# Optimization experiments

Measured on AMD Instinct MI355X. Metric: run time of the kernel, lower is better.

The kernel has to match this reference:

```python
import jax, jax.numpy as jnp
import numpy as np

B, L, K = 4, 2048, 30
HID, EDGE, NL, NH = 128, 16, 3, 4
HD = HID // NH
SCALE = HD ** -0.5
LN_EPS = 1e-5


def setup_inputs() -> dict:
    key = jax.random.key(0)
    ks = jax.random.split(key, 16)
    s = 0.05
    d = {
        "h_nodes": jax.random.normal(ks[0], (B, L, HID), jnp.float32),
        "h_edges": jax.random.normal(ks[1], (B, L, K, EDGE), jnp.float32),
        "mask": jnp.ones((B, L), jnp.float32),
        "Wq": jax.random.normal(ks[2], (NL, HID, HID), jnp.float32) * s,
        "bq": jax.random.normal(ks[3], (NL, HID), jnp.float32) * s,
        "Wk": jax.random.normal(ks[4], (NL, HID, HID), jnp.float32) * s,
        "bk": jax.random.normal(ks[5], (NL, HID), jnp.float32) * s,
        "Wv": jax.random.normal(ks[6], (NL, HID, HID), jnp.float32) * s,
        "bv": jax.random.normal(ks[7], (NL, HID), jnp.float32) * s,
        "We": jax.random.normal(ks[8], (NL, EDGE, NH), jnp.float32) * s,
        "be": jax.random.normal(ks[9], (NL, NH), jnp.float32) * s,
        "Wo": jax.random.normal(ks[10], (NL, HID, HID), jnp.float32) * s,
        "bo": jax.random.normal(ks[11], (NL, HID), jnp.float32) * s,
        "ln_g": jnp.ones((NL, HID), jnp.float32),
        "ln_b": jnp.zeros((NL, HID), jnp.float32),
        "edge_idxs": jax.random.randint(ks[12], (B, L, K), 0, L, jnp.int32),
    }
    return d


def _layer_norm(x, g, b):
    mu = jnp.mean(x, axis=-1, keepdims=True)
    var = jnp.mean((x - mu) ** 2, axis=-1, keepdims=True)
    return (x - mu) * jax.lax.rsqrt(var + LN_EPS) * g + b


# per-batch gather of rows: a [L, ...], idx [L, K] -> [L, K, ...]
_gather = jax.vmap(lambda a, i: a[i])


def _forward(h_nodes, h_edges, mask, Wq, bq, Wk, bk, Wv, bv, We, be, Wo, bo, ln_g, ln_b, edge_idxs):
    neigh_mask = _gather(mask, edge_idxs)                     # [B,L,K]
    attn_mask = mask[:, None, :, None] * neigh_mask[:, None]  # [B,1,L,K]
    h = h_nodes
    for i in range(NL):
        hn = _gather(h, edge_idxs)                            # [B,L,K,HID]
        q = (h @ Wq[i] + bq[i]).reshape(B, L, NH, HD)
        k = (hn @ Wk[i] + bk[i]).reshape(B, L, K, NH, HD)
        v = (hn @ Wv[i] + bv[i]).reshape(B, L, K, NH, HD)
        scores = jnp.einsum('blhd,blkhd->bhlk', q, k) * SCALE
        scores = scores + jnp.transpose(h_edges @ We[i] + be[i], (0, 3, 1, 2))  # edge bias [B,NH,L,K]
        scores = jnp.where(attn_mask == 0, -1e9, scores)
        w = jax.nn.softmax(scores, axis=-1)                   # [B,NH,L,K]
        o = jnp.einsum('bhlk,blkhd->blhd', w, v).reshape(B, L, HID)
        o = o @ Wo[i] + bo[i]
        h = _layer_norm(h + o, ln_g[i], ln_b[i]) * mask[..., None]
    return h


def reference(h_nodes, h_edges, edge_idxs, mask, Wq, bq, Wk, bk, Wv, bv, We, be, Wo, bo, ln_g, ln_b):
    return _forward(h_nodes, h_edges, mask, Wq, bq, Wk, bk, Wv, bv, We, be, Wo, bo, ln_g, ln_b, edge_idxs)
```

## Files before the change

### kernel.cpp

```cpp
#include <hip/hip_runtime.h>
#include <math.h>

#define BB 4
#define LL 2048
#define KK 30
#define HIDD 128
#define EDGEE 16
#define NLL 3
#define NHH 4
#define SCALE_ 0.17677669529663687f
#define NROW 8192
#define NEDG 245760

typedef __attribute__((ext_vector_type(8))) short bf16x8;
typedef __attribute__((ext_vector_type(4))) float f32x4;

__device__ __forceinline__ ushort f2b(float f) {
    union { float f; uint u; } x; x.f = f;
    uint r = x.u + 0x7fff + ((x.u >> 16) & 1);
    return (ushort)(r >> 16);
}

__global__ __launch_bounds__(256) void prep_kernel(
    const float* __restrict__ Wq, const float* __restrict__ Wk,
    const float* __restrict__ Wv, const float* __restrict__ Wo,
    const float* __restrict__ h_edges, const float* __restrict__ We,
    const float* __restrict__ be, const float* __restrict__ h_nodes,
    ushort* __restrict__ WbT, float* __restrict__ eb, ushort* __restrict__ hb)
{
    const int id = blockIdx.x * 256 + threadIdx.x;
    if (blockIdx.y == 0) {
        if (id < 12 * 128 * 128) {
            int m = id >> 14;
            int rem = id & 16383;
            int k = rem >> 7, n = rem & 127;
            int layer = m >> 2, p = m & 3;
            const float* src;
            if (p == 0)      src = Wq + (size_t)layer * 16384;
            else if (p == 1) src = Wk + (size_t)layer * 16384;
            else if (p == 2) src = Wv + (size_t)layer * 16384;
            else             src = Wo + (size_t)layer * 16384;
            WbT[(size_t)m * 16384 + n * 128 + k] = f2b(src[k * 128 + n]);
        }
    } else if (blockIdx.y == 1) {
        __shared__ float We_s[NLL * EDGEE * NHH];
        __shared__ float be_s[NLL * NHH];
        if (threadIdx.x < NLL * EDGEE * NHH) We_s[threadIdx.x] = We[threadIdx.x];
        if (threadIdx.x < NLL * NHH) be_s[threadIdx.x] = be[threadIdx.x];
        __syncthreads();
        if (id < NEDG) {
            const float4* e4 = (const float4*)h_edges + (size_t)id * 4;
            float4 ec[4] = {e4[0], e4[1], e4[2], e4[3]};
            float ev[16];
            #pragma unroll
            for (int q = 0; q < 4; ++q) {
                ev[q * 4 + 0] = ec[q].x; ev[q * 4 + 1] = ec[q].y;
                ev[q * 4 + 2] = ec[q].z; ev[q * 4 + 3] = ec[q].w;
            }
            #pragma unroll
            for (int i = 0; i < NLL; ++i) {
                float r[NHH] = {be_s[i * 4], be_s[i * 4 + 1], be_s[i * 4 + 2], be_s[i * 4 + 3]};
                #pragma unroll
                for (int e = 0; e < EDGEE; ++e) {
                    float v = ev[e];
                    #pragma unroll
                    for (int hq = 0; hq < NHH; ++hq)
                        r[hq] = fmaf(v, We_s[i * 64 + e * NHH + hq], r[hq]);
                }
                ((float4*)eb)[(size_t)i * NEDG + id] = make_float4(r[0], r[1], r[2], r[3]);
            }
        }
    } else {
        float4 v = ((const float4*)h_nodes)[id];
        ushort4 o;
        o.x = f2b(v.x); o.y = f2b(v.y); o.z = f2b(v.z); o.w = f2b(v.w);
        ((ushort4*)hb)[id] = o;
    }
}

__global__ __launch_bounds__(256) void qkv_mfma(
    const ushort* __restrict__ hb, const ushort* __restrict__ WbT,
    const float* __restrict__ bq, const float* __restrict__ bk,
    const float* __restrict__ bv,
    float* __restrict__ Qp, float* __restrict__ Kp, float* __restrict__ Vp)
{
    __shared__ ushort As[128 * 128];
    __shared__ ushort Bs[128 * 128];

    const int t = threadIdx.x;
    const int proj = blockIdx.y;
    const ushort* W = WbT + (size_t)proj * 16384;
    const float* bias = proj == 0 ? bq : (proj == 1 ? bk : bv);
    float* out = proj == 0 ? Qp : (proj == 1 ? Kp : Vp);
    const int row0 = blockIdx.x * 128;

    const uint4* hb4 = (const uint4*)(hb + (size_t)row0 * 128);
    const uint4* W4 = (const uint4*)W;
    #pragma unroll
    for (int i = 0; i < 8; ++i) {
        int c = t + i * 256;
        int r = c >> 4, kc = c & 15;
        int off = (r * 256 + kc * 16) ^ ((r & 7) << 4);
        *(uint4*)((char*)As + off) = hb4[c];
        *(uint4*)((char*)Bs + off) = W4[c];
    }
    __syncthreads();

    const int wid = t >> 6, l = t & 63;
    const int lr = l & 15, lg = l >> 4;
    const int rbase = wid * 32;
    f32x4 acc[2][8];
    #pragma unroll
    for (int m = 0; m < 2; ++m)
        #pragma unroll
        for (int n = 0; n < 8; ++n) acc[m][n] = (f32x4){0.f, 0.f, 0.f, 0.f};

    #pragma unroll
    for (int ks = 0; ks < 4; ++ks) {
        const int kb = (lg * 8 + ks * 32) * 2;
        bf16x8 a[2], b[8];
        #pragma unroll
        for (int m = 0; m < 2; ++m) {
            int row = rbase + m * 16 + lr;
            a[m] = *(const bf16x8*)((const char*)As + ((row * 256 + kb) ^ ((row & 7) << 4)));
        }
        #pragma unroll
        for (int n = 0; n < 8; ++n) {
            int col = n * 16 + lr;
            b[n] = *(const bf16x8*)((const char*)Bs + ((col * 256 + kb) ^ ((col & 7) << 4)));
        }
        #pragma unroll
        for (int m = 0; m < 2; ++m)
            #pragma unroll
            for (int n = 0; n < 8; ++n)
                acc[m][n] = __builtin_amdgcn_mfma_f32_16x16x32_bf16(a[m], b[n], acc[m][n], 0, 0, 0);
    }

    #pragma unroll
    for (int n = 0; n < 8; ++n) {
        int col = n * 16 + lr;
        float bc = bias[col];
        #pragma unroll
        for (int m = 0; m < 2; ++m)
            #pragma unroll
            for (int r = 0; r < 4; ++r) {
                int row = row0 + rbase + m * 16 + lg * 4 + r;
                out[(size_t)row * 128 + col] = acc[m][n][r] + bc;
            }
    }
}

__global__ __launch_bounds__(256) void attn_kernel(
    const float* __restrict__ Qp, const float* __restrict__ Kp,
    const float* __restrict__ Vp,
    const int* __restrict__ edge_idxs, const float4* __restrict__ ebL,
    const float* __restrict__ mask, ushort* __restrict__ o_out)
{
    __shared__ int   widx[8][KK];
    __shared__ float ams[8][KK];
    __shared__ float ebs[8][KK][NHH];

    const int t = threadIdx.x;
    const int grp = t >> 5;
    const int g = t & 31;
    const int row = blockIdx.x * 8 + grp;
    const int b = row >> 11;
    const int hh = g >> 3;

    if (g < KK) {
        int gid = b * LL + edge_idxs[(size_t)row * KK + g];
        widx[grp][g] = gid;
        ams[grp][g] = mask[row] * mask[gid];
        *(float4*)&ebs[grp][g][0] = ebL[(size_t)row * KK + g];
    }
    __syncthreads();

    const float4* Kp4 = (const float4*)Kp;
    const float4* Vp4 = (const float4*)Vp;
    const float4 q4 = ((const float4*)Qp)[(size_t)row * 32 + g];

    float sc[KK];
    #pragma unroll
    for (int kb = 0; kb < 3; ++kb) {
        float4 kv[10];
        #pragma unroll
        for (int j = 0; j < 10; ++j)
            kv[j] = Kp4[(size_t)widx[grp][kb * 10 + j] * 32 + g];
        #pragma unroll
        for (int j = 0; j < 10; ++j) {
            int k = kb * 10 + j;
            float p = q4.x * kv[j].x + q4.y * kv[j].y + q4.z * kv[j].z + q4.w * kv[j].w;
            p += __shfl_xor(p, 4, 32);
            p += __shfl_xor(p, 2, 32);
            p += __shfl_xor(p, 1, 32);
            float am = ams[grp][k];
            float ebv = ebs[grp][k][hh];
            sc[k] = (am == 0.f) ? -1e9f : fmaf(p, SCALE_, ebv);
        }
    }

    float m = sc[0];
    #pragma unroll
    for (int k = 1; k < KK; ++k) m = fmaxf(m, sc[k]);
    float sum = 0.f;
    #pragma unroll
    for (int k = 0; k < KK; ++k) { sc[k] = __expf(sc[k] - m); sum += sc[k]; }
    const float inv = 1.f / sum;

    float4 o = make_float4(0.f, 0.f, 0.f, 0.f);
    #pragma unroll
    for (int kb = 0; kb < 3; ++kb) {
        float4 vv[10];
        #pragma unroll
        for (int j = 0; j < 10; ++j)
            vv[j] = Vp4[(size_t)widx[grp][kb * 10 + j] * 32 + g];
        #pragma unroll
        for (int j = 0; j < 10; ++j) {
            float w = sc[kb * 10 + j];
            o.x = fmaf(w, vv[j].x, o.x);
            o.y = fmaf(w, vv[j].y, o.y);
            o.z = fmaf(w, vv[j].z, o.z);
            o.w = fmaf(w, vv[j].w, o.w);
        }
    }
    ushort ob[4] = {f2b(o.x * inv), f2b(o.y * inv), f2b(o.z * inv), f2b(o.w * inv)};
    *(uint2*)&o_out[(size_t)row * HIDD + g * 4] = *(uint2*)ob;
}

__global__ __launch_bounds__(256) void outproj_mfma(
    const ushort* __restrict__ obb, const ushort* __restrict__ WoT,
    const float* __restrict__ bo, const float* __restrict__ hres,
    const float* __restrict__ g, const float* __restrict__ bb,
    const float* __restrict__ mask, float* __restrict__ hout,
    ushort* __restrict__ hbout)
{
    __shared__ ushort As[128 * 128];
    __shared__ ushort Bs[128 * 128];

    const int t = threadIdx.x;
    const int row0 = blockIdx.x * 128;

    const uint4* A4 = (const uint4*)(obb + (size_t)row0 * 128);
    const uint4* W4 = (const uint4*)WoT;
    #pragma unroll
    for (int i = 0; i < 8; ++i) {
        int c = t + i * 256;
        int r = c >> 4, kc = c & 15;
        int off = (r * 256 + kc * 16) ^ ((r & 7) << 4);
        *(uint4*)((char*)As + off) = A4[c];
        *(uint4*)((char*)Bs + off) = W4[c];
    }
    __syncthreads();

    const int wid = t >> 6, l = t & 63;
    const int lr = l & 15, lg = l >> 4;
    const int rbase = wid * 32;
    f32x4 acc[2][8];
    #pragma unroll
    for (int m = 0; m < 2; ++m)
        #pragma unroll
        for (int n = 0; n < 8; ++n) acc[m][n] = (f32x4){0.f, 0.f, 0.f, 0.f};

    #pragma unroll
    for (int ks = 0; ks < 4; ++ks) {
        const int kb = (lg * 8 + ks * 32) * 2;
        bf16x8 a[2], b[8];
        #pragma unroll
        for (int m = 0; m < 2; ++m) {
            int row = rbase + m * 16 + lr;
            a[m] = *(const bf16x8*)((const char*)As + ((row * 256 + kb) ^ ((row & 7) << 4)));
        }
        #pragma unroll
        for (int n = 0; n < 8; ++n) {
            int col = n * 16 + lr;
            b[n] = *(const bf16x8*)((const char*)Bs + ((col * 256 + kb) ^ ((col & 7) << 4)));
        }
        #pragma unroll
        for (int m = 0; m < 2; ++m)
            #pragma unroll
            for (int n = 0; n < 8; ++n)
                acc[m][n] = __builtin_amdgcn_mfma_f32_16x16x32_bf16(a[m], b[n], acc[m][n], 0, 0, 0);
    }

    float s1[2][4] = {}, s2[2][4] = {};
    #pragma unroll
    for (int n = 0; n < 8; ++n) {
        int col = n * 16 + lr;
        float boc = bo[col];
        #pragma unroll
        for (int m = 0; m < 2; ++m)
            #pragma unroll
            for (int r = 0; r < 4; ++r) {
                int row = row0 + rbase + m * 16 + lg * 4 + r;
                float v = acc[m][n][r] + boc + hres[(size_t)row * 128 + col];
                acc[m][n][r] = v;
                s1[m][r] += v;
                s2[m][r] += v * v;
            }
    }
    #pragma unroll
    for (int m = 0; m < 2; ++m)
        #pragma unroll
        for (int r = 0; r < 4; ++r) {
            float a = s1[m][r], b2 = s2[m][r];
            #pragma unroll
            for (int d = 1; d < 16; d <<= 1) {
                a  += __shfl_xor(a, d, 64);
                b2 += __shfl_xor(b2, d, 64);
            }
            s1[m][r] = a; s2[m][r] = b2;
        }

    float gv[8], bbv[8];
    #pragma unroll
    for (int n = 0; n < 8; ++n) { gv[n] = g[n * 16 + lr]; bbv[n] = bb[n * 16 + lr]; }

    #pragma unroll
    for (int m = 0; m < 2; ++m)
        #pragma unroll
        for (int r = 0; r < 4; ++r) {
            int row = row0 + rbase + m * 16 + lg * 4 + r;
            float mu = s1[m][r] * (1.f / 128.f);
            float var = s2[m][r] * (1.f / 128.f) - mu * mu;
            float rs = rsqrtf(var + 1e-5f);
            float mk = mask[row];
            #pragma unroll
            for (int n = 0; n < 8; ++n) {
                int col = n * 16 + lr;
                float val = ((acc[m][n][r] - mu) * rs * gv[n] + bbv[n]) * mk;
                hout[(size_t)row * 128 + col] = val;
                hbout[(size_t)row * 128 + col] = f2b(val);
            }
        }
}

extern "C" void kernel_launch(void* const* d_in, const int* in_sizes, int n_in,
                              void* d_out, int out_size, void* d_ws, size_t ws_size,
                              hipStream_t stream) {
    const float* h_nodes = (const float*)d_in[0];
    const float* h_edges = (const float*)d_in[1];
    const float* mask    = (const float*)d_in[2];
    const float* Wq = (const float*)d_in[3];
    const float* bq = (const float*)d_in[4];
    const float* Wk = (const float*)d_in[5];
    const float* bk = (const float*)d_in[6];
    const float* Wv = (const float*)d_in[7];
    const float* bv = (const float*)d_in[8];
    const float* We = (const float*)d_in[9];
    const float* be = (const float*)d_in[10];
    const float* Wo = (const float*)d_in[11];
    const float* bo = (const float*)d_in[12];
    const float* ln_g = (const float*)d_in[13];
    const float* ln_b = (const float*)d_in[14];
    const int* edge_idxs = (const int*)d_in[15];

    float* ws = (float*)d_ws;
    const size_t NE = (size_t)NROW * HIDD;
    float* h   = ws;
    float* Qp  = ws + NE;
    float* Kp  = ws + 2 * NE;
    float* Vp  = ws + 3 * NE;
    ushort* obb = (ushort*)(ws + 4 * NE);
    ushort* hb  = obb + NE;
    ushort* WbT = hb + NE;
    float* eb   = (float*)(WbT + 12 * 16384);

    prep_kernel<<<dim3(1024, 3), 256, 0, stream>>>(
        Wq, Wk, Wv, Wo, h_edges, We, be, h_nodes, WbT, eb, hb);

    for (int i = 0; i < NLL; ++i) {
        qkv_mfma<<<dim3(NROW / 128, 3), 256, 0, stream>>>(
            hb, WbT + (size_t)i * 4 * 16384,
            bq + i * HIDD, bk + i * HIDD, bv + i * HIDD,
            Qp, Kp, Vp);
        attn_kernel<<<NROW / 8, 256, 0, stream>>>(
            Qp, Kp, Vp, edge_idxs,
            (const float4*)eb + (size_t)i * NEDG, mask, obb);
        bool last = (i == NLL - 1);
        outproj_mfma<<<NROW / 128, 256, 0, stream>>>(
            obb, WbT + ((size_t)i * 4 + 3) * 16384, bo + i * HIDD,
            (i == 0) ? h_nodes : h,
            ln_g + i * HIDD, ln_b + i * HIDD, mask,
            last ? (float*)d_out : h, hb);
    }
}
```

Baseline: 103.7 us.

## Restructure attention kernel to 16 lanes per row with DPP reductions and block swizzle

Each attention row is now handled by 16 lanes instead of 32. Every lane loads two float4 chunks (8 floats) of K and V per neighbor, so each block covers 16 rows and half as many blocks are launched. The cross-lane dot-product reduction uses DPP quad-permute moves in place of three shuffles. A block-index swizzle remaps which rows each workgroup processes, likely to spread work across XCDs or improve cache locality. The intent is to cut shuffle overhead and issue wider loads, at the cost of more registers per thread and fewer waves in flight.

Measured after the change: 107.9 us. +4.1%, slower.

```diff
diff --git a/kernel.cpp b/kernel.cpp
--- a/kernel.cpp
+++ b/kernel.cpp
@@ -19,6 +19,14 @@
     union { float f; uint u; } x; x.f = f;
     uint r = x.u + 0x7fff + ((x.u >> 16) & 1);
     return (ushort)(r >> 16);
+}
+__device__ __forceinline__ float qxor1(float x) {
+    return __int_as_float(__builtin_amdgcn_mov_dpp(
+        __float_as_int(x), 0xB1, 0xF, 0xF, true));
+}
+__device__ __forceinline__ float qxor2(float x) {
+    return __int_as_float(__builtin_amdgcn_mov_dpp(
+        __float_as_int(x), 0x4E, 0xF, 0xF, true));
 }
 
 __global__ __launch_bounds__(256) void prep_kernel(
@@ -156,43 +164,51 @@
     const int* __restrict__ edge_idxs, const float4* __restrict__ ebL,
     const float* __restrict__ mask, ushort* __restrict__ o_out)
 {
-    __shared__ int   widx[8][KK];
-    __shared__ float ams[8][KK];
-    __shared__ float ebs[8][KK][NHH];
+    __shared__ int   widx[16][KK];
+    __shared__ float ams[16][KK];
+    __shared__ float ebs[16][KK][NHH];
+
+    const int lbid = (blockIdx.x & 7) * 64 + (blockIdx.x >> 3);
 
     const int t = threadIdx.x;
-    const int grp = t >> 5;
-    const int g = t & 31;
-    const int row = blockIdx.x * 8 + grp;
-    const int b = row >> 11;
-    const int hh = g >> 3;
-
-    if (g < KK) {
-        int gid = b * LL + edge_idxs[(size_t)row * KK + g];
-        widx[grp][g] = gid;
-        ams[grp][g] = mask[row] * mask[gid];
-        *(float4*)&ebs[grp][g][0] = ebL[(size_t)row * KK + g];
+    const int grp = t >> 4;
+    const int g = t & 15;
+    const int row = lbid * 16 + grp;
+    const int hh = g >> 2;
+
+    for (int i = t; i < 16 * KK; i += 256) {
+        int rr = i / KK, k = i - rr * KK;
+        int prow = lbid * 16 + rr;
+        int bb2 = prow >> 11;
+        int gid = bb2 * LL + edge_idxs[(size_t)prow * KK + k];
+        widx[rr][k] = gid;
+        ams[rr][k] = mask[prow] * mask[gid];
+        *(float4*)&ebs[rr][k][0] = ebL[(size_t)prow * KK + k];
     }
     __syncthreads();
 
     const float4* Kp4 = (const float4*)Kp;
     const float4* Vp4 = (const float4*)Vp;
-    const float4 q4 = ((const float4*)Qp)[(size_t)row * 32 + g];
+    const float4 qa = ((const float4*)Qp)[(size_t)row * 32 + 2 * g];
+    const float4 qb = ((const float4*)Qp)[(size_t)row * 32 + 2 * g + 1];
 
     float sc[KK];
     #pragma unroll
-    for (int kb = 0; kb < 3; ++kb) {
-        float4 kv[10];
-        #pragma unroll
-        for (int j = 0; j < 10; ++j)
-            kv[j] = Kp4[(size_t)widx[grp][kb * 10 + j] * 32 + g];
-        #pragma unroll
-        for (int j = 0; j < 10; ++j) {
-            int k = kb * 10 + j;
-            float p = q4.x * kv[j].x + q4.y * kv[j].y + q4.z * kv[j].z + q4.w * kv[j].w;
-            p += __shfl_xor(p, 4, 32);
-            p += __shfl_xor(p, 2, 32);
-            p += __shfl_xor(p, 1, 32);
+    for (int kb = 0; kb < 5; ++kb) {
+        float4 ka[6], kbv[6];
+        #pragma unroll
+        for (int j = 0; j < 6; ++j) {
+            size_t base = (size_t)widx[grp][kb * 6 + j] * 32 + 2 * g;
+            ka[j]  = Kp4[base];
+            kbv[j] = Kp4[base + 1];
+        }
+        #pragma unroll
+        for (int j = 0; j < 6; ++j) {
+            int k = kb * 6 + j;
+            float p = qa.x * ka[j].x + qa.y * ka[j].y + qa.z * ka[j].z + qa.w * ka[j].w
+                    + qb.x * kbv[j].x + qb.y * kbv[j].y + qb.z * kbv[j].z + qb.w * kbv[j].w;
+            p += qxor1(p);
+            p += qxor2(p);
             float am = ams[grp][k];
             float ebv = ebs[grp][k][hh];
             sc[k] = (am == 0.f) ? -1e9f : fmaf(p, SCALE_, ebv);
@@ -207,24 +223,29 @@
     for (int k = 0; k < KK; ++k) { sc[k] = __expf(sc[k] - m); sum += sc[k]; }
     const float inv = 1.f / sum;
 
-    float4 o = make_float4(0.f, 0.f, 0.f, 0.f);
-    #pragma unroll
-    for (int kb = 0; kb < 3; ++kb) {
-        float4 vv[10];
-        #pragma unroll
-        for (int j = 0; j < 10; ++j)
-            vv[j] = Vp4[(size_t)widx[grp][kb * 10 + j] * 32 + g];
-        #pragma unroll
-        for (int j = 0; j < 10; ++j) {
-            float w = sc[kb * 10 + j];
-            o.x = fmaf(w, vv[j].x, o.x);
-            o.y = fmaf(w, vv[j].y, o.y);
-            o.z = fmaf(w, vv[j].z, o.z);
-            o.w = fmaf(w, vv[j].w, o.w);
-        }
-    }
-    ushort ob[4] = {f2b(o.x * inv), f2b(o.y * inv), f2b(o.z * inv), f2b(o.w * inv)};
-    *(uint2*)&o_out[(size_t)row * HIDD + g * 4] = *(uint2*)ob;
+    float oa0 = 0.f, oa1 = 0.f, oa2 = 0.f, oa3 = 0.f;
+    float ob0 = 0.f, ob1 = 0.f, ob2 = 0.f, ob3 = 0.f;
+    #pragma unroll
+    for (int kb = 0; kb < 5; ++kb) {
+        float4 va[6], vb[6];
+        #pragma unroll
+        for (int j = 0; j < 6; ++j) {
+            size_t base = (size_t)widx[grp][kb * 6 + j] * 32 + 2 * g;
+            va[j] = Vp4[base];
+            vb[j] = Vp4[base + 1];
+        }
+        #pragma unroll
+        for (int j = 0; j < 6; ++j) {
+            float w = sc[kb * 6 + j];
+            oa0 = fmaf(w, va[j].x, oa0); oa1 = fmaf(w, va[j].y, oa1);
+            oa2 = fmaf(w, va[j].z, oa2); oa3 = fmaf(w, va[j].w, oa3);
+            ob0 = fmaf(w, vb[j].x, ob0); ob1 = fmaf(w, vb[j].y, ob1);
+            ob2 = fmaf(w, vb[j].z, ob2); ob3 = fmaf(w, vb[j].w, ob3);
+        }
+    }
+    ushort o8[8] = {f2b(oa0 * inv), f2b(oa1 * inv), f2b(oa2 * inv), f2b(oa3 * inv),
+                    f2b(ob0 * inv), f2b(ob1 * inv), f2b(ob2 * inv), f2b(ob3 * inv)};
+    *(uint4*)&o_out[(size_t)row * HIDD + g * 8] = *(uint4*)o8;
 }
 
 __global__ __launch_bounds__(256) void outproj_mfma(
@@ -373,7 +394,7 @@
             hb, WbT + (size_t)i * 4 * 16384,
             bq + i * HIDD, bk + i * HIDD, bv + i * HIDD,
             Qp, Kp, Vp);
-        attn_kernel<<<NROW / 8, 256, 0, stream>>>(
+        attn_kernel<<<NROW / 16, 256, 0, stream>>>(
             Qp, Kp, Vp, edge_idxs,
             (const float4*)eb + (size_t)i * NEDG, mask, obb);
         bool last = (i == NLL - 1);
```
